# Kernel tuning notes

Measured on AMD Instinct MI355X. Metric: run time of the kernel, lower is better.

The kernel has to match this reference:

```python
import jax, jax.numpy as jnp
import numpy as np

N, E, H, HEADS, L = 10000, 64000, 128, 8, 8
D = H // HEADS
CUTOFF = 5.0
EPS = 1e-5


def _xavier(key, shape):
    lim = float(np.sqrt(6.0 / (shape[0] + shape[1])))
    return jax.random.uniform(key, shape, minval=-lim, maxval=lim, dtype=jnp.float32)


def setup_inputs() -> dict:
    key = jax.random.key(0)
    ks = jax.random.split(key, 20)
    zeros = lambda *s: jnp.zeros(s, jnp.float32)
    return {
        "x": jax.random.normal(ks[0], (N, H), jnp.float32),
        "vec": 0.1 * jax.random.normal(ks[1], (N, L, H), jnp.float32),
        "f_ij": jax.random.normal(ks[2], (E, H), jnp.float32),
        "d_ij": jax.random.normal(ks[3], (E, L), jnp.float32),
        "r_ij": jax.random.uniform(ks[4], (E,), jnp.float32, 0.0, CUTOFF),
        "edge_index": jax.random.randint(ks[5], (2, E), 0, N),
        "ln_g": jnp.ones((H,), jnp.float32), "ln_b": zeros(H),
        "vln_w": jnp.ones((H,), jnp.float32),
        "W_vec": _xavier(ks[6], (H, 3 * H)),
        "W_q": _xavier(ks[7], (H, H)), "b_q": zeros(H),
        "W_k": _xavier(ks[8], (H, H)), "b_k": zeros(H),
        "W_v": _xavier(ks[9], (H, H)), "b_v": zeros(H),
        "W_dk": _xavier(ks[10], (H, H)), "b_dk": zeros(H),
        "W_dv": _xavier(ks[11], (H, H)), "b_dv": zeros(H),
        "W_s": _xavier(ks[12], (H, 2 * H)), "b_s": zeros(2 * H),
        "W_f": _xavier(ks[13], (H, H)), "b_f": zeros(H),
        "W_src": _xavier(ks[14], (H, H)),
        "W_trg": _xavier(ks[15], (H, H)),
        "W_o": _xavier(ks[16], (H, 3 * H)), "b_o": zeros(3 * H),
    }


def _layernorm(x, g, b):
    mu = jnp.mean(x, -1, keepdims=True)
    var = jnp.mean((x - mu) ** 2, -1, keepdims=True)
    return (x - mu) * jax.lax.rsqrt(var + EPS) * g + b


def _cutoff(r):
    # CosineCutoff: 0.5*(cos(pi*r/cutoff)+1) for r < cutoff
    return 0.5 * (jnp.cos(jnp.pi * r / CUTOFF) + 1.0) * (r < CUTOFF).astype(r.dtype)


def _vec_rejection(v, d):
    # v: [E, L, H], d: [E, L]; remove the component of v along d (per channel)
    proj = jnp.einsum("elh,el->eh", v, d)
    return v - proj[:, None, :] * d[:, :, None]


def reference(x, vec, f_ij, d_ij, r_ij, edge_index, ln_g, ln_b, vln_w, W_vec,
              W_q, b_q, W_k, b_k, W_v, b_v, W_dk, b_dk, W_dv, b_dv,
              W_s, b_s, W_f, b_f, W_src, W_trg, W_o, b_o):
    src, dst = edge_index[0], edge_index[1]  # j (source), i (target)
    x = _layernorm(x, ln_g, ln_b)
    vec = vec * vln_w  # VecLayerNorm with norm_type="none": identity norm * weight

    q = (x @ W_q + b_q).reshape(N, HEADS, D)
    k = (x @ W_k + b_k).reshape(N, HEADS, D)
    v = (x @ W_v + b_v).reshape(N, HEADS, D)
    dk = jax.nn.silu(f_ij @ W_dk + b_dk).reshape(E, HEADS, D)
    dv = jax.nn.silu(f_ij @ W_dv + b_dv).reshape(E, HEADS, D)

    vec1, vec2, vec3 = jnp.split(jnp.einsum("nlh,hk->nlk", vec, W_vec), 3, axis=-1)
    vec_dot = jnp.sum(vec1 * vec2, axis=1)  # [N, H]

    # ---- message (per edge) ----
    attn = jnp.sum(q[dst] * k[src] * dk, axis=-1)          # [E, HEADS]
    attn = jax.nn.silu(attn) * _cutoff(r_ij)[:, None]
    vm = (v[src] * dv * attn[:, :, None]).reshape(E, H)    # [E, H]
    s1, s2 = jnp.split(jax.nn.silu(vm @ W_s + b_s), 2, axis=-1)
    vec_m = vec[src] * s1[:, None, :] + s2[:, None, :] * d_ij[:, :, None]  # [E, L, H]

    # ---- aggregate (scatter-add to target nodes) ----
    x_agg = jax.ops.segment_sum(vm, dst, num_segments=N)       # [N, H]
    vec_agg = jax.ops.segment_sum(vec_m, dst, num_segments=N)  # [N, L, H]

    # ---- edge update ----
    w1 = _vec_rejection(jnp.einsum("elh,hk->elk", vec[dst], W_trg), d_ij)
    w2 = _vec_rejection(jnp.einsum("elh,hk->elk", vec[src], W_src), -d_ij)
    w_dot = jnp.sum(w1 * w2, axis=1)                       # [E, H]
    df_ij = jax.nn.silu(f_ij @ W_f + b_f) * w_dot

    # ---- node update ----
    o1, o2, o3 = jnp.split(x_agg @ W_o + b_o, 3, axis=-1)
    dx = vec_dot * o2 + o3
    dvec = vec3 * o1[:, None, :] + vec_agg
    return dx, dvec, df_ij
```

## Files before the change

kernel.cpp:

```cpp
#include <hip/hip_runtime.h>
#include <hip/hip_bf16.h>
#include <math.h>

#define N_NODES 10000
#define N_EDGES 64000
#define H 128
#define L 8
#define NL (N_NODES * L)

typedef __attribute__((ext_vector_type(4))) float f32x4;
typedef __attribute__((ext_vector_type(8))) __bf16 bf16x8;

__device__ __forceinline__ float silu_f(float x) { return x / (1.f + __expf(-x)); }

__global__ __launch_bounds__(256) void ln_kernel(const float* __restrict__ x,
                                                 const float* __restrict__ g,
                                                 const float* __restrict__ b,
                                                 __bf16* __restrict__ out, int n_nodes) {
  int wave = threadIdx.x >> 6;
  int lane = threadIdx.x & 63;
  int n = blockIdx.x * 4 + wave;
  if (n >= n_nodes) return;
  const float* xr = x + (size_t)n * H;
  float a0 = xr[lane], a1 = xr[lane + 64];
  float s = a0 + a1;
#pragma unroll
  for (int off = 32; off >= 1; off >>= 1) s += __shfl_xor(s, off, 64);
  float mu = s * (1.f / H);
  float d0 = a0 - mu, d1 = a1 - mu;
  float v = d0 * d0 + d1 * d1;
#pragma unroll
  for (int off = 32; off >= 1; off >>= 1) v += __shfl_xor(v, off, 64);
  float rstd = rsqrtf(v * (1.f / H) + 1e-5f);
  __bf16* orow = out + (size_t)n * H;
  orow[lane] = (__bf16)(d0 * rstd * g[lane] + b[lane]);
  orow[lane + 64] = (__bf16)(d1 * rstd * g[lane + 64] + b[lane + 64]);
}

__global__ __launch_bounds__(256) void vecw_kernel(const float* __restrict__ vec,
                                                   const float* __restrict__ w,
                                                   __bf16* __restrict__ out, size_t total8) {
  size_t i = (size_t)blockIdx.x * blockDim.x + threadIdx.x;
  size_t stride = (size_t)gridDim.x * blockDim.x;
  for (; i < total8; i += stride) {
    size_t base = i * 8;
    f32x4 a = *(const f32x4*)(vec + base);
    f32x4 b = *(const f32x4*)(vec + base + 4);
    int c = (int)(base & 127);
    bf16x8 h;
    h[0] = (__bf16)(a[0] * w[c + 0]); h[1] = (__bf16)(a[1] * w[c + 1]);
    h[2] = (__bf16)(a[2] * w[c + 2]); h[3] = (__bf16)(a[3] * w[c + 3]);
    h[4] = (__bf16)(b[0] * w[c + 4]); h[5] = (__bf16)(b[1] * w[c + 5]);
    h[6] = (__bf16)(b[2] * w[c + 6]); h[7] = (__bf16)(b[3] * w[c + 7]);
    *(bf16x8*)(out + base) = h;
  }
}

__global__ __launch_bounds__(256) void f2b_kernel(const float* __restrict__ in,
                                                  __bf16* __restrict__ out, size_t total8) {
  size_t i = (size_t)blockIdx.x * blockDim.x + threadIdx.x;
  size_t stride = (size_t)gridDim.x * blockDim.x;
  for (; i < total8; i += stride) {
    size_t base = i * 8;
    f32x4 a = *(const f32x4*)(in + base);
    f32x4 b = *(const f32x4*)(in + base + 4);
    bf16x8 h;
    h[0] = (__bf16)a[0]; h[1] = (__bf16)a[1]; h[2] = (__bf16)a[2]; h[3] = (__bf16)a[3];
    h[4] = (__bf16)b[0]; h[5] = (__bf16)b[1]; h[6] = (__bf16)b[2]; h[7] = (__bf16)b[3];
    *(bf16x8*)(out + base) = h;
  }
}

__global__ __launch_bounds__(256) void wconv_kernel(
    const float* __restrict__ Wvec, const float* __restrict__ Wq, const float* __restrict__ Wk,
    const float* __restrict__ Wv, const float* __restrict__ Wdk, const float* __restrict__ Wdv,
    const float* __restrict__ Ws, const float* __restrict__ Wtrg, const float* __restrict__ Wsrc,
    const float* __restrict__ Wf, const float* __restrict__ Wo,
    const float* __restrict__ bq, const float* __restrict__ bk, const float* __restrict__ bv,
    const float* __restrict__ bdk, const float* __restrict__ bdv, const float* __restrict__ bf,
    __bf16* __restrict__ Wt, float* __restrict__ bqkv, float* __restrict__ bfm) {
  int bid = blockIdx.x;
  int t = threadIdx.x;
  if (bid >= 256) {
    if (bid == 256) {
      if (t < 128) { bqkv[t] = bq[t]; bqkv[128 + t] = bk[t]; bqkv[256 + t] = bv[t]; }
    } else {
      if (t < 128) { bfm[t] = bdk[t]; bfm[128 + t] = bdv[t]; bfm[256 + t] = bf[t]; }
    }
    return;
  }
  int ct = bid >> 2, kt = bid & 3;
  int gc0 = ct * 32;
  const float* W; int ldw, sc0;
  if      (gc0 < 384)  { W = Wvec; ldw = 384; sc0 = gc0; }
  else if (gc0 < 512)  { W = Wtrg; ldw = 128; sc0 = gc0 - 384; }
  else if (gc0 < 640)  { W = Wsrc; ldw = 128; sc0 = gc0 - 512; }
  else if (gc0 < 768)  { W = Wq;   ldw = 128; sc0 = gc0 - 640; }
  else if (gc0 < 896)  { W = Wk;   ldw = 128; sc0 = gc0 - 768; }
  else if (gc0 < 1024) { W = Wv;   ldw = 128; sc0 = gc0 - 896; }
  else if (gc0 < 1152) { W = Wdk;  ldw = 128; sc0 = gc0 - 1024; }
  else if (gc0 < 1280) { W = Wdv;  ldw = 128; sc0 = gc0 - 1152; }
  else if (gc0 < 1408) { W = Wf;   ldw = 128; sc0 = gc0 - 1280; }
  else if (gc0 < 1664) { W = Ws;   ldw = 256; sc0 = gc0 - 1408; }
  else                 { W = Wo;   ldw = 384; sc0 = gc0 - 1664; }
  __shared__ float tile[32][33];
  int tx = t & 31, ty = t >> 5;
#pragma unroll
  for (int i = 0; i < 4; ++i)
    tile[ty + i * 8][tx] = W[(size_t)(kt * 32 + ty + i * 8) * ldw + sc0 + tx];
  __syncthreads();
#pragma unroll
  for (int i = 0; i < 4; ++i)
    Wt[(size_t)(gc0 + ty + i * 8) * 128 + kt * 32 + tx] = (__bf16)tile[tx][ty + i * 8];
}

__global__ __launch_bounds__(256, 2) void vdot_gemm(const __bf16* __restrict__ A,
                                                    const __bf16* __restrict__ Bt,
                                                    float* __restrict__ vdot) {
  __shared__ __bf16 As[128 * 128];
  const int tid = threadIdx.x;
  const int lane = tid & 63;
  const int wave = tid >> 6;
  const int wm = wave >> 1, wn = wave & 1;
  const int row0 = blockIdx.x * 128;

#pragma unroll
  for (int i = 0; i < 8; ++i) {
    int c = tid + i * 256;
    int row = c >> 4, k8 = c & 15;
    int k8s = k8 ^ (row & 7);
    const __bf16* src = A + (size_t)(row0 + row) * 128 + k8s * 8;
    __builtin_amdgcn_global_load_lds((const __attribute__((address_space(1))) void*)src,
                                     (__attribute__((address_space(3))) void*)(As + c * 8),
                                     16, 0, 0);
  }
  __syncthreads();

  f32x4 pacc[4][4], acc[4][4];
#pragma unroll
  for (int mi = 0; mi < 4; ++mi)
#pragma unroll
    for (int ni = 0; ni < 4; ++ni) {
      pacc[mi][ni] = f32x4{0.f, 0.f, 0.f, 0.f};
      acc[mi][ni] = f32x4{0.f, 0.f, 0.f, 0.f};
    }
#pragma unroll
  for (int ct = 0; ct < 2; ++ct) {
    const __bf16* Bbase =
        Bt + ((size_t)(ct * 128 + wn * 64 + (lane & 15)) << 7) + ((lane >> 4) << 3);
#pragma unroll
    for (int ks = 0; ks < 4; ++ks) {
      bf16x8 b[4];
#pragma unroll
      for (int ni = 0; ni < 4; ++ni) b[ni] = *(const bf16x8*)(Bbase + (ni << 11) + (ks << 5));
      bf16x8 a[4];
#pragma unroll
      for (int mi = 0; mi < 4; ++mi) {
        int row = wm * 64 + mi * 16 + (lane & 15);
        int byte = (row * 256 + ks * 64 + ((lane >> 4) << 4)) ^ ((row & 7) << 4);
        a[mi] = *(const bf16x8*)((const char*)As + byte);
      }
      if (ct == 0) {
#pragma unroll
        for (int mi = 0; mi < 4; ++mi)
#pragma unroll
          for (int ni = 0; ni < 4; ++ni)
            pacc[mi][ni] =
                __builtin_amdgcn_mfma_f32_16x16x32_bf16(a[mi], b[ni], pacc[mi][ni], 0, 0, 0);
      } else {
#pragma unroll
        for (int mi = 0; mi < 4; ++mi)
#pragma unroll
          for (int ni = 0; ni < 4; ++ni)
            acc[mi][ni] =
                __builtin_amdgcn_mfma_f32_16x16x32_bf16(a[mi], b[ni], acc[mi][ni], 0, 0, 0);
      }
    }
  }
#pragma unroll
  for (int mi = 0; mi < 4; ++mi) {
#pragma unroll
    for (int ni = 0; ni < 4; ++ni) {
      float sr = pacc[mi][ni][0] * acc[mi][ni][0] + pacc[mi][ni][1] * acc[mi][ni][1] +
                 pacc[mi][ni][2] * acc[mi][ni][2] + pacc[mi][ni][3] * acc[mi][ni][3];
      sr += __shfl_xor(sr, 16, 64);
      if ((lane & 16) == 0) {
        int node = (row0 >> 3) + wm * 8 + mi * 2 + (lane >> 5);
        int col = wn * 64 + ni * 16 + (lane & 15);
        vdot[(size_t)node * 128 + col] = sr;
      }
    }
  }
}

template <typename CT>
__global__ __launch_bounds__(256, 3) void gemm_v9(const __bf16* __restrict__ A,
                                                  const __bf16* __restrict__ Bt,
                                                  const float* __restrict__ bias,
                                                  CT* __restrict__ C, int M, int nx, int ny,
                                                  int ldc, int act) {
  __shared__ __bf16 As[128 * 128];
  __bf16* Cs = As;
  const int bid = blockIdx.x;
  const int xi = bid & 7;
  const int rem = bid >> 3;
  const int y = rem % ny;
  const int x = (rem / ny) * 8 + xi;
  if (x >= nx) return;
  const int tid = threadIdx.x;
  const int lane = tid & 63;
  const int wave = tid >> 6;
  const int wm = wave >> 1, wn = wave & 1;
  const int row0 = x * 128;

#pragma unroll
  for (int i = 0; i < 8; ++i) {
    int c = tid + i * 256;
    int row = c >> 4, k8 = c & 15;
    int k8s = k8 ^ (row & 7);
    const __bf16* src = A + (size_t)(row0 + row) * 128 + k8s * 8;
    __builtin_amdgcn_global_load_lds((const __attribute__((address_space(1))) void*)src,
                                     (__attribute__((address_space(3))) void*)(As + c * 8),
                                     16, 0, 0);
  }
  __syncthreads();

  const __bf16* Bbase =
      Bt + ((size_t)(y * 128 + wn * 64 + (lane & 15)) << 7) + ((lane >> 4) << 3);
  bf16x8 b[4][4];
#pragma unroll
  for (int ks = 0; ks < 4; ++ks)
#pragma unroll
    for (int ni = 0; ni < 4; ++ni) b[ks][ni] = *(const bf16x8*)(Bbase + (ni << 11) + (ks << 5));

  f32x4 acc[4][4];
#pragma unroll
  for (int mi = 0; mi < 4; ++mi)
#pragma unroll
    for (int ni = 0; ni < 4; ++ni) acc[mi][ni] = f32x4{0.f, 0.f, 0.f, 0.f};

#pragma unroll
  for (int ks = 0; ks < 4; ++ks) {
    bf16x8 a[4];
#pragma unroll
    for (int mi = 0; mi < 4; ++mi) {
      int row = wm * 64 + mi * 16 + (lane & 15);
      int byte = (row * 256 + ks * 64 + ((lane >> 4) << 4)) ^ ((row & 7) << 4);
      a[mi] = *(const bf16x8*)((const char*)As + byte);
    }
#pragma unroll
    for (int mi = 0; mi < 4; ++mi)
#pragma unroll
      for (int ni = 0; ni < 4; ++ni)
        acc[mi][ni] =
            __builtin_amdgcn_mfma_f32_16x16x32_bf16(a[mi], b[ks][ni], acc[mi][ni], 0, 0, 0);
  }

  const int cstore = y * 128;
  if constexpr (sizeof(CT) == 2) {
#pragma unroll
    for (int p = 0; p < 2; ++p) {
      __syncthreads();
      int rl = (wm << 5) | ((lane >> 4) << 2);
#pragma unroll
      for (int q = 0; q < 2; ++q) {
        int mi = 2 * p + q;
#pragma unroll
        for (int ni = 0; ni < 4; ++ni) {
          int col = wn * 64 + ni * 16 + (lane & 15);
          float bv = bias ? bias[cstore + col] : 0.f;
#pragma unroll
          for (int r = 0; r < 4; ++r) {
            float xv = acc[mi][ni][r] + bv;
            if (act) xv = silu_f(xv);
            Cs[(rl + q * 16 + r) * 136 + col] = (__bf16)xv;
          }
        }
      }
      __syncthreads();
#pragma unroll
      for (int rr = 0; rr < 4; ++rr) {
        int row = (tid >> 4) + rr * 16;
        int chunk = tid & 15;
        bf16x8 v = *(const bf16x8*)(Cs + row * 136 + chunk * 8);
        int grow = row0 + (row >> 5) * 64 + (2 * p + ((row >> 4) & 1)) * 16 + (row & 15);
        if (grow < M)
          *(bf16x8*)(C + (size_t)grow * ldc + cstore + chunk * 8) = v;
      }
    }
  } else {
#pragma unroll
    for (int mi = 0; mi < 4; ++mi) {
      int rbase = row0 + wm * 64 + mi * 16 + ((lane >> 4) << 2);
#pragma unroll
      for (int ni = 0; ni < 4; ++ni) {
        int gcol = cstore + wn * 64 + ni * 16 + (lane & 15);
        float bv = bias ? bias[cstore + wn * 64 + ni * 16 + (lane & 15)] : 0.f;
#pragma unroll
        for (int r = 0; r < 4; ++r) {
          int grow = rbase + r;
          if (grow < M) {
            float xv = acc[mi][ni][r] + bv;
            if (act) xv = silu_f(xv);
            C[(size_t)grow * ldc + gcol] = (CT)xv;
          }
        }
      }
    }
  }
}

static inline int swz_grid(int nx, int ny) { return ((nx + 7) / 8) * ny * 8; }

__global__ __launch_bounds__(256) void msg_kernel(const __bf16* __restrict__ qkv,
                                                  const __bf16* __restrict__ fm,
                                                  const float* __restrict__ r_ij,
                                                  const int* __restrict__ ei,
                                                  const int* __restrict__ elist,
                                                  __bf16* __restrict__ vm) {
  int p = blockIdx.x * 2 + (threadIdx.x >> 7);
  int h = threadIdx.x & 127;
  int e = elist[p];
  int src = ei[e], dst = ei[N_EDGES + e];
  float qv = (float)qkv[(size_t)dst * 384 + h];
  float kv = (float)qkv[(size_t)src * 384 + 128 + h];
  float vv = (float)qkv[(size_t)src * 384 + 256 + h];
  float t = qv * kv * (float)fm[(size_t)e * 384 + h];
#pragma unroll
  for (int off = 8; off >= 1; off >>= 1) t += __shfl_xor(t, off, 16);
  float r = r_ij[e];
  float cut = 0.5f * (__cosf(0.6283185307f * r) + 1.f);
  cut = (r < 5.f) ? cut : 0.f;
  float attn = silu_f(t) * cut;
  vm[(size_t)e * H + h] = (__bf16)(vv * (float)fm[(size_t)e * 384 + 128 + h] * attn);
}

__global__ __launch_bounds__(256) void hist_kernel(const int* __restrict__ ei,
                                                   int* __restrict__ cnt) {
  int e = blockIdx.x * 256 + threadIdx.x;
  if (e < N_EDGES) atomicAdd(&cnt[ei[N_EDGES + e]], 1);
}

__global__ __launch_bounds__(1024) void scan_kernel(const int* __restrict__ cnt,
                                                    int* __restrict__ rowptr) {
  __shared__ int wsum[16];
  int t = threadIdx.x;
  int base = t * 10;
  int local[10];
  int s = 0;
#pragma unroll
  for (int i = 0; i < 10; ++i) {
    int v = (base + i < N_NODES) ? cnt[base + i] : 0;
    local[i] = s;
    s += v;
  }
  int lane = t & 63, wave = t >> 6;
  int inc = s;
#pragma unroll
  for (int off = 1; off < 64; off <<= 1) {
    int u = __shfl_up(inc, off, 64);
    if (lane >= off) inc += u;
  }
  if (lane == 63) wsum[wave] = inc;
  __syncthreads();
  if (t == 0) {
    int acc = 0;
#pragma unroll
    for (int w = 0; w < 16; ++w) { int v = wsum[w]; wsum[w] = acc; acc += v; }
  }
  __syncthreads();
  int excl = inc - s + wsum[wave];
#pragma unroll
  for (int i = 0; i < 10; ++i)
    if (base + i <= N_NODES) rowptr[base + i] = excl + local[i];
}

__global__ __launch_bounds__(256) void fill_kernel(const int* __restrict__ ei,
                                                   const int* __restrict__ rowptr,
                                                   int* __restrict__ cursor,
                                                   int* __restrict__ elist) {
  int e = blockIdx.x * 256 + threadIdx.x;
  if (e < N_EDGES) {
    int d = ei[N_EDGES + e];
    int p = atomicAdd(&cursor[d], 1);
    elist[rowptr[d] + p] = e;
  }
}

__global__ __launch_bounds__(256) void gather_kernel(const __bf16* __restrict__ vm,
                                                     const __bf16* __restrict__ s,
                                                     const __bf16* __restrict__ vecw,
                                                     const float* __restrict__ d_ij,
                                                     const int* __restrict__ ei,
                                                     const int* __restrict__ rowptr,
                                                     const int* __restrict__ elist,
                                                     __bf16* __restrict__ x_agg,
                                                     float* __restrict__ dvec) {
  int n = blockIdx.x * 2 + (threadIdx.x >> 7);
  int h = threadIdx.x & 127;
  if (n >= N_NODES) return;
  int beg = rowptr[n], end = rowptr[n + 1];
  float ax = 0.f;
  float av[L] = {};
  for (int p = beg; p < end; ++p) {
    int e = elist[p];
    int src = ei[e];
    ax += (float)vm[(size_t)e * H + h];
    float s1 = (float)s[(size_t)e * 256 + h];
    float s2 = (float)s[(size_t)e * 256 + 128 + h];
    const __bf16* vrow = vecw + (size_t)src * L * H + h;
    const float* dd = d_ij + (size_t)e * L;
#pragma unroll
    for (int l = 0; l < L; l++) av[l] += (float)vrow[l * H] * s1 + s2 * dd[l];
  }
  x_agg[(size_t)n * H + h] = (__bf16)ax;
  float* drow = dvec + (size_t)n * L * H + h;
#pragma unroll
  for (int l = 0; l < L; l++) drow[l * H] = av[l];
}

__global__ __launch_bounds__(256) void edgeupd_kernel(const __bf16* __restrict__ big,
                                                      const float* __restrict__ d_ij,
                                                      const __bf16* __restrict__ fm,
                                                      const int* __restrict__ ei,
                                                      const int* __restrict__ elist,
                                                      float* __restrict__ df) {
  int p = blockIdx.x * 2 + (threadIdx.x >> 7);
  int h = threadIdx.x & 127;
  int e = elist[p];
  int src = ei[e], dst = ei[N_EDGES + e];
  float d[L];
  float sd2 = 0.f;
#pragma unroll
  for (int l = 0; l < L; l++) {
    d[l] = d_ij[(size_t)e * L + l];
    sd2 += d[l] * d[l];
  }
  const __bf16* arow = big + (size_t)dst * 8 * 384 + 128 + h;
  const __bf16* brow = big + (size_t)src * 8 * 384 + 256 + h;
  float dot = 0.f, p1 = 0.f, p2 = 0.f;
#pragma unroll
  for (int l = 0; l < L; l++) {
    float a = (float)arow[l * 384], bb = (float)brow[l * 384];
    dot += a * bb;
    p1 += a * d[l];
    p2 += bb * d[l];
  }
  float wdot = dot - p1 * p2 * (2.f - sd2);
  df[(size_t)e * H + h] = (float)fm[(size_t)e * 384 + 256 + h] * wdot;
}

__global__ __launch_bounds__(256) void final_kernel(const float* __restrict__ o,
                                                    const float* __restrict__ vdot,
                                                    const __bf16* __restrict__ big,
                                                    float* __restrict__ dx,
                                                    float* __restrict__ dvec, int n_nodes) {
  int n = blockIdx.x * 2 + (threadIdx.x >> 7);
  int h = threadIdx.x & 127;
  if (n >= n_nodes) return;
  float o1 = o[(size_t)n * 384 + h];
  float o2 = o[(size_t)n * 384 + 128 + h];
  float o3 = o[(size_t)n * 384 + 256 + h];
  dx[(size_t)n * H + h] = vdot[(size_t)n * H + h] * o2 + o3;
  float* drow = dvec + (size_t)n * L * H + h;
  const __bf16* v3 = big + (size_t)n * 8 * 384 + h;
#pragma unroll
  for (int l = 0; l < L; l++) drow[l * H] += (float)v3[l * 384] * o1;
}

extern "C" void kernel_launch(void* const* d_in, const int* in_sizes, int n_in, void* d_out,
                              int out_size, void* d_ws, size_t ws_size, hipStream_t stream) {
  const float* x = (const float*)d_in[0];
  const float* vec = (const float*)d_in[1];
  const float* f_ij = (const float*)d_in[2];
  const float* d_ij = (const float*)d_in[3];
  const float* r_ij = (const float*)d_in[4];
  const int* ei = (const int*)d_in[5];
  const float* ln_g = (const float*)d_in[6];
  const float* ln_b = (const float*)d_in[7];
  const float* vln_w = (const float*)d_in[8];
  const float* W_vec = (const float*)d_in[9];
  const float* W_q = (const float*)d_in[10];
  const float* b_q = (const float*)d_in[11];
  const float* W_k = (const float*)d_in[12];
  const float* b_k = (const float*)d_in[13];
  const float* W_v = (const float*)d_in[14];
  const float* b_v = (const float*)d_in[15];
  const float* W_dk = (const float*)d_in[16];
  const float* b_dk = (const float*)d_in[17];
  const float* W_dv = (const float*)d_in[18];
  const float* b_dv = (const float*)d_in[19];
  const float* W_s = (const float*)d_in[20];
  const float* b_s = (const float*)d_in[21];
  const float* W_f = (const float*)d_in[22];
  const float* b_f = (const float*)d_in[23];
  const float* W_src = (const float*)d_in[24];
  const float* W_trg = (const float*)d_in[25];
  const float* W_o = (const float*)d_in[26];
  const float* b_o = (const float*)d_in[27];

  float* out = (float*)d_out;
  float* dx = out;
  float* dvec = out + (size_t)N_NODES * H;
  float* df = dvec + (size_t)N_NODES * L * H;

  float* ws = (float*)d_ws;
  __bf16* vecw = (__bf16*)ws;
  __bf16* big = (__bf16*)(ws + 5120000);
  __bf16* fm = (__bf16*)(ws + 20480000);
  __bf16* vm = (__bf16*)(ws + 32768000);
  __bf16* s_buf = (__bf16*)(ws + 36864000);
  __bf16* qkv = (__bf16*)(ws + 45056000);
  __bf16* xln = (__bf16*)(ws + 48896000);
  __bf16* xagg = (__bf16*)(ws + 49536000);
  float* vdot = ws + 50176000;
  __bf16* Wt = (__bf16*)(ws + 51456000);
  float* bqkv = ws + 51456000 + 131072;
  float* bfm = bqkv + 384;
  int* rowptr = (int*)(bfm + 384);
  int* elist = rowptr + 10001;
  int* cnt = elist + 64000;
  int* cursor = cnt + 10000;
  __bf16* fijb = (__bf16*)(ws + 51800000);

  float* o_buf = ws + 45056000;

  dim3 b256(256);

  hipMemsetAsync(cnt, 0, N_NODES * sizeof(int), stream);
  hipMemsetAsync(cursor, 0, N_NODES * sizeof(int), stream);
  hist_kernel<<<dim3((N_EDGES + 255) / 256), b256, 0, stream>>>(ei, cnt);
  scan_kernel<<<dim3(1), dim3(1024), 0, stream>>>(cnt, rowptr);
  fill_kernel<<<dim3((N_EDGES + 255) / 256), b256, 0, stream>>>(ei, rowptr, cursor, elist);

  wconv_kernel<<<dim3(258), b256, 0, stream>>>(W_vec, W_q, W_k, W_v, W_dk, W_dv, W_s, W_trg,
                                               W_src, W_f, W_o, b_q, b_k, b_v, b_dk, b_dv, b_f,
                                               Wt, bqkv, bfm);
  f2b_kernel<<<dim3(2048), b256, 0, stream>>>(f_ij, fijb, (size_t)N_EDGES * H / 8);
  ln_kernel<<<dim3((N_NODES + 3) / 4), b256, 0, stream>>>(x, ln_g, ln_b, xln, N_NODES);
  vecw_kernel<<<dim3(2048), b256, 0, stream>>>(vec, vln_w, vecw, (size_t)NL * H / 8);
  vdot_gemm<<<dim3(625), b256, 0, stream>>>(vecw, Wt, vdot);
  gemm_v9<__bf16><<<dim3(swz_grid(625, 3)), b256, 0, stream>>>(
      vecw, Wt + (size_t)256 * 128, nullptr, big, NL, 625, 3, 384, 0);
  gemm_v9<__bf16><<<dim3(swz_grid(79, 3)), b256, 0, stream>>>(
      xln, Wt + (size_t)640 * 128, bqkv, qkv, N_NODES, 79, 3, 384, 0);
  gemm_v9<__bf16><<<dim3(swz_grid(500, 3)), b256, 0, stream>>>(
      fijb, Wt + (size_t)1024 * 128, bfm, fm, N_EDGES, 500, 3, 384, 1);
  msg_kernel<<<dim3(N_EDGES / 2), b256, 0, stream>>>(qkv, fm, r_ij, ei, elist, vm);
  gemm_v9<__bf16><<<dim3(swz_grid(500, 2)), b256, 0, stream>>>(
      vm, Wt + (size_t)1408 * 128, b_s, s_buf, N_EDGES, 500, 2, 256, 1);
  gather_kernel<<<dim3(N_NODES / 2), b256, 0, stream>>>(vm, s_buf, vecw, d_ij, ei, rowptr,
                                                        elist, xagg, dvec);
  edgeupd_kernel<<<dim3(N_EDGES / 2), b256, 0, stream>>>(big, d_ij, fm, ei, elist, df);
  gemm_v9<float><<<dim3(swz_grid(79, 3)), b256, 0, stream>>>(
      xagg, Wt + (size_t)1664 * 128, b_o, o_buf, N_NODES, 79, 3, 384, 0);
  final_kernel<<<dim3(5000), b256, 0, stream>>>(o_buf, vdot, big, dx, dvec, N_NODES);
}
```

Before: 325.7 us.

## Fuse edge-update computation into per-node gather kernel

Merges the separate edge-update kernel into the destination-node gather loop, so the target-side projected vector rows for a node are loaded once into registers and reused across all its incoming edges. d_ij and the source-side loads happen in the same pass as the aggregation. This removes one launch and the repeated per-edge reload of the dst rows. In exchange, per-node work becomes more serial and load imbalance across nodes with differing degree may grow, with fewer blocks (5000 vs 32000) to hide latency.

```diff
diff --git a/kernel.cpp b/kernel.cpp
--- a/kernel.cpp
+++ b/kernel.cpp
@@ -387,67 +387,62 @@
   }
 }
 
-__global__ __launch_bounds__(256) void gather_kernel(const __bf16* __restrict__ vm,
-                                                     const __bf16* __restrict__ s,
-                                                     const __bf16* __restrict__ vecw,
-                                                     const float* __restrict__ d_ij,
-                                                     const int* __restrict__ ei,
-                                                     const int* __restrict__ rowptr,
-                                                     const int* __restrict__ elist,
-                                                     __bf16* __restrict__ x_agg,
-                                                     float* __restrict__ dvec) {
+__global__ __launch_bounds__(256) void node_kernel(const __bf16* __restrict__ vm,
+                                                   const __bf16* __restrict__ s,
+                                                   const __bf16* __restrict__ vecw,
+                                                   const __bf16* __restrict__ big,
+                                                   const __bf16* __restrict__ fm,
+                                                   const float* __restrict__ d_ij,
+                                                   const int* __restrict__ ei,
+                                                   const int* __restrict__ rowptr,
+                                                   const int* __restrict__ elist,
+                                                   __bf16* __restrict__ x_agg,
+                                                   float* __restrict__ dvec,
+                                                   float* __restrict__ df) {
   int n = blockIdx.x * 2 + (threadIdx.x >> 7);
   int h = threadIdx.x & 127;
   if (n >= N_NODES) return;
   int beg = rowptr[n], end = rowptr[n + 1];
+
+  float vt[L];
+  const __bf16* trow = big + (size_t)n * 8 * 384 + 128 + h;
+#pragma unroll
+  for (int l = 0; l < L; l++) vt[l] = (float)trow[l * 384];
+
   float ax = 0.f;
   float av[L] = {};
   for (int p = beg; p < end; ++p) {
     int e = elist[p];
     int src = ei[e];
+    const float* dd = d_ij + (size_t)e * L;
+    float d[L], sd2 = 0.f;
+#pragma unroll
+    for (int l = 0; l < L; l++) {
+      d[l] = dd[l];
+      sd2 += d[l] * d[l];
+    }
     ax += (float)vm[(size_t)e * H + h];
     float s1 = (float)s[(size_t)e * 256 + h];
     float s2 = (float)s[(size_t)e * 256 + 128 + h];
     const __bf16* vrow = vecw + (size_t)src * L * H + h;
-    const float* dd = d_ij + (size_t)e * L;
-#pragma unroll
-    for (int l = 0; l < L; l++) av[l] += (float)vrow[l * H] * s1 + s2 * dd[l];
+    const __bf16* brow = big + (size_t)src * 8 * 384 + 256 + h;
+    float dot = 0.f, p1 = 0.f, p2 = 0.f;
+#pragma unroll
+    for (int l = 0; l < L; l++) {
+      float vw = (float)vrow[l * H];
+      av[l] += vw * s1 + s2 * d[l];
+      float bb = (float)brow[l * 384];
+      dot += vt[l] * bb;
+      p1 += vt[l] * d[l];
+      p2 += bb * d[l];
+    }
+    float wdot = dot - p1 * p2 * (2.f - sd2);
+    df[(size_t)e * H + h] = (float)fm[(size_t)e * 384 + 256 + h] * wdot;
   }
   x_agg[(size_t)n * H + h] = (__bf16)ax;
   float* drow = dvec + (size_t)n * L * H + h;
 #pragma unroll
   for (int l = 0; l < L; l++) drow[l * H] = av[l];
-}
-
-__global__ __launch_bounds__(256) void edgeupd_kernel(const __bf16* __restrict__ big,
-                                                      const float* __restrict__ d_ij,
-                                                      const __bf16* __restrict__ fm,
-                                                      const int* __restrict__ ei,
-                                                      const int* __restrict__ elist,
-                                                      float* __restrict__ df) {
-  int p = blockIdx.x * 2 + (threadIdx.x >> 7);
-  int h = threadIdx.x & 127;
-  int e = elist[p];
-  int src = ei[e], dst = ei[N_EDGES + e];
-  float d[L];
-  float sd2 = 0.f;
-#pragma unroll
-  for (int l = 0; l < L; l++) {
-    d[l] = d_ij[(size_t)e * L + l];
-    sd2 += d[l] * d[l];
-  }
-  const __bf16* arow = big + (size_t)dst * 8 * 384 + 128 + h;
-  const __bf16* brow = big + (size_t)src * 8 * 384 + 256 + h;
-  float dot = 0.f, p1 = 0.f, p2 = 0.f;
-#pragma unroll
-  for (int l = 0; l < L; l++) {
-    float a = (float)arow[l * 384], bb = (float)brow[l * 384];
-    dot += a * bb;
-    p1 += a * d[l];
-    p2 += bb * d[l];
-  }
-  float wdot = dot - p1 * p2 * (2.f - sd2);
-  df[(size_t)e * H + h] = (float)fm[(size_t)e * 384 + 256 + h] * wdot;
 }
 
 __global__ __launch_bounds__(256) void final_kernel(const float* __restrict__ o,
@@ -549,9 +544,8 @@
   msg_kernel<<<dim3(N_EDGES / 2), b256, 0, stream>>>(qkv, fm, r_ij, ei, elist, vm);
   gemm_v9<__bf16><<<dim3(swz_grid(500, 2)), b256, 0, stream>>>(
       vm, Wt + (size_t)1408 * 128, b_s, s_buf, N_EDGES, 500, 2, 256, 1);
-  gather_kernel<<<dim3(N_NODES / 2), b256, 0, stream>>>(vm, s_buf, vecw, d_ij, ei, rowptr,
-                                                        elist, xagg, dvec);
-  edgeupd_kernel<<<dim3(N_EDGES / 2), b256, 0, stream>>>(big, d_ij, fm, ei, elist, df);
+  node_kernel<<<dim3(N_NODES / 2), b256, 0, stream>>>(vm, s_buf, vecw, big, fm, d_ij, ei,
+                                                      rowptr, elist, xagg, dvec, df);
   gemm_v9<float><<<dim3(swz_grid(79, 3)), b256, 0, stream>>>(
       xagg, Wt + (size_t)1664 * 128, b_o, o_buf, N_NODES, 79, 3, 384, 0);
   final_kernel<<<dim3(5000), b256, 0, stream>>>(o_buf, vdot, big, dx, dvec, N_NODES);
```

Measured after the change: 321.5 us. Within noise of the previous version (-1.3%).
